# Kernel optimization log

Hardware: AMD Instinct MI355X
Metric: run time of the kernel (lower is better)

## Reference

```python
import jax, jax.numpy as jnp
import numpy as np

N, IN, M = 8192, 512, 512


def setup_inputs() -> dict:
    key = jax.random.key(0)
    ks = jax.random.split(key, 16)
    sI = 1.0 / np.sqrt(IN)
    sM = 1.0 / np.sqrt(M)
    def p(k, shape, scale):
        return jax.random.uniform(k, shape, jnp.float32, -scale, scale)
    # topologically sorted tree: parent[i] < i for i>0; root (i=0) points to sentinel N
    rng = np.random.default_rng(0)
    parent = (rng.random(N) * np.arange(N)).astype(np.int64)
    parent[0] = N
    return {
        "inputs": jax.random.normal(ks[0], (N, IN), jnp.float32),
        "parent": jnp.asarray(parent),
        # FPChildSumTreeLSTM params (bottom-up)
        "cs_Wx": p(ks[1], (5 * M, IN), sI), "cs_bx": p(ks[2], (5 * M,), sI),
        "cs_Wio": p(ks[3], (2 * M, M), sM), "cs_bio": p(ks[4], (2 * M,), sM),
        "cs_Wfz": p(ks[5], (2 * M, M), sM), "cs_bfz": p(ks[6], (2 * M,), sM),
        "cs_Wum": p(ks[7], (M, M), sM), "cs_bum": p(ks[8], (M,), sM),
        # FPChainTreeLSTM params (top-down)
        "ch_Wx": p(ks[9], (5 * M, IN), sI), "ch_bx": p(ks[10], (5 * M,), sI),
        "ch_Wh": p(ks[11], (4 * M, M), sM), "ch_bh": p(ks[12], (4 * M,), sM),
        "ch_Wum": p(ks[13], (M, M), sM), "ch_bum": p(ks[14], (M,), sM),
    }


def _childsum(inputs, parent, Wx, bx, Wio, bio, Wfz, bfz, Wum, bum):
    # Precompute input projections for all nodes at once; row N is a zero sentinel.
    px = inputs @ Wx.T + bx                                  # (N, 5M)
    px = jnp.concatenate([px, jnp.zeros((1, 5 * M), px.dtype)], axis=0)
    ix, fx, ox, zx, ux = (px[:, j * M:(j + 1) * M] for j in range(5))
    # Process nodes leaves->root (reverse topo order). Each finished node j
    # scatters its parent-dependent contributions into accumulators at parent[j]:
    #   acc_h  += h_j
    #   acc_fc += sigmoid(fx_parent + U_f h_j + b_f) * c_j
    #   acc_zc += sigmoid(zx_parent + U_z h_j + b_z) * tanh(c_j)
    # Leaves see zero accumulators, which exactly matches the torch zero phantom child.
    zero = jnp.zeros((N + 1, M), inputs.dtype)

    def step(carry, i):
        acc_h, acc_fc, acc_zc = carry
        io = acc_h[i] @ Wio.T + bio                          # (2M,)
        i_g = jax.nn.sigmoid(ix[i] + io[:M])
        o_g = jax.nn.sigmoid(ox[i] + io[M:])
        u = jnp.tanh(ux[i] + acc_zc[i] @ Wum.T + bum)
        c = i_g * u + acc_fc[i]
        h = o_g * jnp.tanh(c)
        p = parent[i]                                        # root -> sentinel N
        fz = h @ Wfz.T + bfz
        f = jax.nn.sigmoid(fx[p] + fz[:M])
        z = jax.nn.sigmoid(zx[p] + fz[M:])
        acc_h = acc_h.at[p].add(h)
        acc_fc = acc_fc.at[p].add(f * c)
        acc_zc = acc_zc.at[p].add(z * jnp.tanh(c))
        return (acc_h, acc_fc, acc_zc), h

    _, hs = jax.lax.scan(step, (zero, zero, zero), jnp.arange(N - 1, -1, -1))
    return hs[-1]                                            # root hidden, (M,)


def _chain(inputs, parent, Wx, bx, Wh, bh, Wum, bum):
    qx = inputs @ Wx.T + bx                                  # (N, 5M), order i,o,f,z,u
    ix, ox, fx, zx, ux = (qx[:, j * M:(j + 1) * M] for j in range(5))
    zero = jnp.zeros((N + 1, M), inputs.dtype)               # slot N = root's zero parent

    def step(carry, i):
        c_all, h_all = carry
        p = parent[i]
        pc, ph = c_all[p], h_all[p]
        g = ph @ Wh.T + bh                                   # (4M,), order i,o,f,z
        i_g = jax.nn.sigmoid(ix[i] + g[:M])
        o_g = jax.nn.sigmoid(ox[i] + g[M:2 * M])
        f_g = jax.nn.sigmoid(fx[i] + g[2 * M:3 * M])
        z_g = jax.nn.sigmoid(zx[i] + g[3 * M:])
        u = jnp.tanh(ux[i] + (z_g * jnp.tanh(pc)) @ Wum.T + bum)
        c = i_g * u + f_g * pc
        h = o_g * jnp.tanh(c)
        return (c_all.at[i].set(c), h_all.at[i].set(h)), None

    (_, h_all), _ = jax.lax.scan(step, (zero, zero), jnp.arange(N))
    return jnp.max(h_all[:N], axis=0)                        # max over all node hiddens, (M,)


def reference(inputs, parent, cs_Wx, cs_bx, cs_Wio, cs_bio, cs_Wfz, cs_bfz,
              cs_Wum, cs_bum, ch_Wx, ch_bx, ch_Wh, ch_bh, ch_Wum, ch_bum):
    frep = _childsum(inputs, parent, cs_Wx, cs_bx, cs_Wio, cs_bio,
                     cs_Wfz, cs_bfz, cs_Wum, cs_bum)
    brep = _chain(inputs, parent, ch_Wx, ch_bx, ch_Wh, ch_bh, ch_Wum, ch_bum)
    return jnp.concatenate([frep, brep])[None, :]            # (1, 2M)
```

## Files before the change

### kernel.cpp

```cpp
#include <hip/hip_runtime.h>
#include <hip/hip_cooperative_groups.h>
#include <hip/hip_bf16.h>

typedef unsigned short u16;
typedef unsigned int u32;
typedef unsigned long long u64;

#define NN 8192
#define PXC 2560
#define MAXD 36
#define GY 64
#define GYM 32

typedef __attribute__((ext_vector_type(8))) short bf16x8;
typedef __attribute__((ext_vector_type(4))) float f32x4;

static constexpr size_t SZ_PX  = (size_t)(NN + 1) * PXC * 2;
static constexpr size_t SZ_ACC = (size_t)(NN + 1) * 512 * 4;
static constexpr size_t SZ_HB  = (size_t)(NN + 1) * 512 * 2;
static constexpr size_t SZ_G   = (size_t)(NN + 1) * 1536 * 4;
static constexpr size_t SZ_NW  = (size_t)5242880 * 2;

static constexpr size_t OFF_PX    = 0;
static constexpr size_t OFF_QX    = OFF_PX + SZ_PX;
static constexpr size_t OFF_ACCH  = OFF_QX + SZ_PX;
static constexpr size_t OFF_ACCF  = OFF_ACCH + SZ_ACC;
static constexpr size_t OFF_ACCZ  = OFF_ACCF + SZ_ACC;
static constexpr size_t OFF_C     = OFF_ACCZ + SZ_ACC;
static constexpr size_t OFF_HB    = OFF_C + SZ_ACC;
static constexpr size_t OFF_ZB    = OFF_HB + SZ_HB;
static constexpr size_t OFF_G     = OFF_ZB + SZ_HB;
static constexpr size_t OFF_NW    = OFF_G + SZ_G;
static constexpr size_t OFF_DEPTH = OFF_NW + SZ_NW;
static constexpr size_t OFF_ORDER = OFF_DEPTH + (size_t)NN * 4;
static constexpr size_t OFF_MISC  = OFF_ORDER + (size_t)NN * 4;
static constexpr size_t OFF_LVL   = OFF_MISC + 1024;
static constexpr size_t OFF_NB    = OFF_LVL + 512;
static constexpr size_t OFF_PN    = OFF_NB + 20480;
static constexpr size_t OFF_PMAX  = OFF_PN + (size_t)NN * 4;
static constexpr size_t OFF_BAR   = OFF_PMAX + (size_t)128 * 512 * 4;
static constexpr size_t WS_TOTAL  = OFF_BAR + 32768;

#define NW_CSWX  0
#define NW_CHWX  1310720
#define NW_CSWIO 2621440
#define NW_CSWFZ 3145728
#define NW_CSWUM 3670016
#define NW_CHWH  3932160
#define NW_CHWUM 4980736

#define NB_CSBX  0
#define NB_CSBIO 2560
#define NB_CSBFZ 3584
#define NB_CSBUM 4608
#define NB_CHBX  5120
#define NB_CHBH  7680
#define NB_CHBUM 9728

__device__ __forceinline__ float bfu(u16 u) { return __uint_as_float(((u32)u) << 16); }
__device__ __forceinline__ u16 f2bf(float f) {
    u32 u = __float_as_uint(f);
    u += 0x7fffu + ((u >> 16) & 1u);
    return (u16)(u >> 16);
}
__device__ __forceinline__ float sigf(float x) {
    x = fminf(fmaxf(x, -30.f), 30.f);
    return 1.f / (1.f + __expf(-x));
}
__device__ __forceinline__ float tanhq(float x) {
    x = fminf(fmaxf(x, -15.f), 15.f);
    return 1.f - 2.f / (__expf(2.f * x) + 1.f);
}
__device__ __forceinline__ bf16x8 cvt8(const float* p) {
    float4 a = *(const float4*)p;
    float4 b = *(const float4*)(p + 4);
    union { u32 u[4]; bf16x8 v; } r;
    r.u[0] = ((__float_as_uint(a.x) + 0x8000u) >> 16) | ((__float_as_uint(a.y) + 0x8000u) & 0xffff0000u);
    r.u[1] = ((__float_as_uint(a.z) + 0x8000u) >> 16) | ((__float_as_uint(a.w) + 0x8000u) & 0xffff0000u);
    r.u[2] = ((__float_as_uint(b.x) + 0x8000u) >> 16) | ((__float_as_uint(b.y) + 0x8000u) & 0xffff0000u);
    r.u[3] = ((__float_as_uint(b.z) + 0x8000u) >> 16) | ((__float_as_uint(b.w) + 0x8000u) & 0xffff0000u);
    return r.v;
}

__device__ __forceinline__ u64 cld64(const void* p) {
    return __hip_atomic_load((const u64*)p, __ATOMIC_RELAXED, __HIP_MEMORY_SCOPE_AGENT);
}
__device__ __forceinline__ float cldf(const float* p) {
    return __hip_atomic_load(p, __ATOMIC_RELAXED, __HIP_MEMORY_SCOPE_AGENT);
}
__device__ __forceinline__ void cstf(float* p, float v) {
    __hip_atomic_store(p, v, __ATOMIC_RELAXED, __HIP_MEMORY_SCOPE_AGENT);
}
__device__ __forceinline__ void cst16(u16* p, u16 v) {
    __hip_atomic_store(p, v, __ATOMIC_RELAXED, __HIP_MEMORY_SCOPE_AGENT);
}
__device__ __forceinline__ bf16x8 cvt8a(const float* p) {
    union { u64 u; u32 w[2]; } a, b, c, d;
    a.u = cld64(p); b.u = cld64(p + 2); c.u = cld64(p + 4); d.u = cld64(p + 6);
    union { u32 u[4]; bf16x8 v; } r;
    r.u[0] = ((a.w[0] + 0x8000u) >> 16) | ((a.w[1] + 0x8000u) & 0xffff0000u);
    r.u[1] = ((b.w[0] + 0x8000u) >> 16) | ((b.w[1] + 0x8000u) & 0xffff0000u);
    r.u[2] = ((c.w[0] + 0x8000u) >> 16) | ((c.w[1] + 0x8000u) & 0xffff0000u);
    r.u[3] = ((d.w[0] + 0x8000u) >> 16) | ((d.w[1] + 0x8000u) & 0xffff0000u);
    return r.v;
}

__device__ __forceinline__ void grid_bar(u32* B, int bid, u32 tgt) {
    __syncthreads();
    int tid = threadIdx.x;
    if (tid == 0)
        __hip_atomic_store(B + 16 + bid * 16, tgt, __ATOMIC_RELAXED, __HIP_MEMORY_SCOPE_AGENT);
    if (blockIdx.x == 0) {
        if (tid < 256) {
            while (__hip_atomic_load(B + 16 + tid * 16, __ATOMIC_RELAXED, __HIP_MEMORY_SCOPE_AGENT) < tgt)
                __builtin_amdgcn_s_sleep(2);
        }
        __syncthreads();
        if (tid == 0)
            __hip_atomic_store(B, tgt, __ATOMIC_RELAXED, __HIP_MEMORY_SCOPE_AGENT);
    }
    if (tid == 0) {
        while (__hip_atomic_load(B, __ATOMIC_RELAXED, __HIP_MEMORY_SCOPE_AGENT) < tgt)
            __builtin_amdgcn_s_sleep(2);
        asm volatile("" ::: "memory");
    }
    __syncthreads();
}

__device__ __forceinline__ void mini_bar(u32* MF, int cgi, u32 tgt) {
    __syncthreads();
    if (threadIdx.x == 0) {
        __hip_atomic_store(MF + cgi * 4, tgt, __ATOMIC_RELAXED, __HIP_MEMORY_SCOPE_AGENT);
        for (;;) {
            u32 a = __hip_atomic_load(MF + 0,  __ATOMIC_RELAXED, __HIP_MEMORY_SCOPE_AGENT);
            u32 b = __hip_atomic_load(MF + 4,  __ATOMIC_RELAXED, __HIP_MEMORY_SCOPE_AGENT);
            u32 c = __hip_atomic_load(MF + 8,  __ATOMIC_RELAXED, __HIP_MEMORY_SCOPE_AGENT);
            u32 d = __hip_atomic_load(MF + 12, __ATOMIC_RELAXED, __HIP_MEMORY_SCOPE_AGENT);
            if (a >= tgt && b >= tgt && c >= tgt && d >= tgt) break;
            __builtin_amdgcn_s_sleep(1);
        }
        asm volatile("" ::: "memory");
    }
    __syncthreads();
}

__global__ void k_detect(const u32* __restrict__ fin, const u32* __restrict__ pin,
                         int* __restrict__ fcnt, int* __restrict__ pcnt,
                         u32* __restrict__ barz) {
    int i = blockIdx.x * 256 + threadIdx.x;
    if (i < 8192) barz[i] = 0u;
    if (i < 4096) {
        u32 w = fin[i];
        int e = (w >> 7) & 0xFF;
        if (w != 0u && e >= 0x70 && e <= 0x8F) atomicAdd(fcnt, 1);
    }
    if (i >= 1 && i < 4096) {
        if (pin[2 * i - 1] != 0u) atomicAdd(pcnt, 1);
    }
}

__global__ void k_pnorm_depth(const u32* __restrict__ pin, const int* __restrict__ pcnt,
                              int* __restrict__ pnorm, int* __restrict__ depth,
                              u16* __restrict__ HB, float* __restrict__ Call) {
    int i = blockIdx.x * 256 + threadIdx.x;
    if (i < 512) {
        HB[(size_t)NN * 512 + i] = 0;
        Call[(size_t)NN * 512 + i] = 0.f;
    }
    if (i >= NN) return;
    bool is64 = (*pcnt < 100);
    int p = (int)(is64 ? pin[2 * i] : pin[i]);
    pnorm[i] = p;
    int d = 0;
    while (p != NN && p >= 0 && p < NN && d < 9000) {
        d++;
        p = (int)(is64 ? pin[2 * p] : pin[p]);
    }
    depth[i] = d;
}

__global__ __launch_bounds__(1024) void k_levels(const int* __restrict__ depth,
                                                 int* __restrict__ lvl, int* __restrict__ order) {
    __shared__ int cnts[64];
    __shared__ int cur[64];
    int t = threadIdx.x;
    if (t < 64) cnts[t] = 0;
    __syncthreads();
    for (int i = t; i < NN; i += 1024) {
        int d = depth[i]; if (d > 63) d = 63;
        atomicAdd(&cnts[d], 1);
    }
    __syncthreads();
    if (t == 0) {
        int s = 0; lvl[0] = 0;
        for (int d = 0; d < 64; ++d) { cur[d] = s; s += cnts[d]; lvl[d + 1] = s; }
        int D = 1;
        for (int d = 63; d >= 0; --d) if (cnts[d] > 0) { D = d + 1; break; }
        lvl[80] = D;
    }
    __syncthreads();
    for (int i = t; i < NN; i += 1024) {
        int d = depth[i]; if (d > 63) d = 63;
        int pos = atomicAdd(&cur[d], 1);
        order[pos] = i;
    }
}

struct NormSrcs { const void* p[15]; };
__global__ __launch_bounds__(256) void k_norm_all(NormSrcs s, u16* __restrict__ NGI,
                                                  u16* __restrict__ NW, u16* __restrict__ NB,
                                                  const int* __restrict__ fcnt) {
    const int cum[16] = {0, 1048576, 1376256, 1703936, 1835008, 1966080, 2031616, 2293760,
                         2359296, 2359936, 2360192, 2360448, 2360576, 2361216, 2361728, 2361856};
    const int dof[15] = {0, NW_CSWX / 4, NW_CHWX / 4, NW_CSWIO / 4, NW_CSWFZ / 4, NW_CSWUM / 4,
                         NW_CHWH / 4, NW_CHWUM / 4, NB_CSBX / 4, NB_CSBIO / 4, NB_CSBFZ / 4,
                         NB_CSBUM / 4, NB_CHBX / 4, NB_CHBH / 4, NB_CHBUM / 4};
    bool isbf = (*fcnt > 2048);
    int total = 2361856;
    int istart = isbf ? cum[8] : 0;
    for (int i = istart + blockIdx.x * 256 + threadIdx.x; i < total; i += gridDim.x * 256) {
        int seg = 0;
#pragma unroll
        for (int k = 1; k < 15; ++k) if (i >= cum[k]) seg = k;
        int off = i - cum[seg];
        u16* dbase = (seg == 0) ? NGI : (seg < 8 ? NW : NB);
        ushort4* dst = (ushort4*)dbase + dof[seg] + off;
        if (isbf) {
            *dst = ((const ushort4*)s.p[seg])[off];
        } else {
            float4 v = ((const float4*)s.p[seg])[off];
            ushort4 o; o.x = f2bf(v.x); o.y = f2bf(v.y); o.z = f2bf(v.z); o.w = f2bf(v.w);
            *dst = o;
        }
    }
}

#define ASTR 528
__global__ __launch_bounds__(256) void k_gemm_in(
    const u16* __restrict__ Ao, const u16* __restrict__ An,
    const u16* __restrict__ Wcs_o, const u16* __restrict__ Wcs_n,
    const u16* __restrict__ Wch_o, const u16* __restrict__ Wch_n,
    const u16* __restrict__ bcs, const u16* __restrict__ bch,
    u16* __restrict__ Ccs, u16* __restrict__ Cch,
    const int* __restrict__ fcnt)
{
    __shared__ __align__(16) u16 AS[64 * ASTR];
    bool isbf = (*fcnt > 2048);
    int z = blockIdx.z;
    const u16* A = isbf ? Ao : An;
    const u16* W = z ? (isbf ? Wch_o : Wch_n) : (isbf ? Wcs_o : Wcs_n);
    const u16* bias = z ? bch : bcs;
    u16* C = z ? Cch : Ccs;

    int m0 = blockIdx.y * 64;
    for (int e = threadIdx.x; e < 64 * 64; e += 256) {
        int row = e >> 6, c8 = e & 63;
        *(uint4*)&AS[row * ASTR + c8 * 8] = *(const uint4*)(A + (size_t)(m0 + row) * 512 + c8 * 8);
    }
    __syncthreads();

    int wv = threadIdx.x >> 6;
    int lane = threadIdx.x & 63;
    int r = lane & 15, q = lane >> 4;
    int n0 = blockIdx.x * 256 + wv * 64;
    const u16* pb[4];
#pragma unroll
    for (int jt = 0; jt < 4; ++jt) pb[jt] = W + (size_t)(n0 + jt * 16 + r) * 512 + q * 8;
    f32x4 acc[4][4] = {};
#pragma unroll 2
    for (int k0 = 0; k0 < 512; k0 += 32) {
        bf16x8 a[4], b[4];
#pragma unroll
        for (int mi = 0; mi < 4; ++mi)
            a[mi] = *(const bf16x8*)&AS[(mi * 16 + r) * ASTR + k0 + q * 8];
#pragma unroll
        for (int jt = 0; jt < 4; ++jt) b[jt] = *(const bf16x8*)(pb[jt] + k0);
#pragma unroll
        for (int mi = 0; mi < 4; ++mi)
#pragma unroll
            for (int jt = 0; jt < 4; ++jt)
                acc[mi][jt] = __builtin_amdgcn_mfma_f32_16x16x32_bf16(a[mi], b[jt], acc[mi][jt], 0, 0, 0);
    }
#pragma unroll
    for (int jt = 0; jt < 4; ++jt) {
        int c = n0 + jt * 16 + r;
        float bv = bfu(bias[c]);
#pragma unroll
        for (int mi = 0; mi < 4; ++mi) {
            size_t b0 = (size_t)(m0 + mi * 16 + q * 4) * PXC + c;
#pragma unroll
            for (int i = 0; i < 4; ++i)
                C[b0 + (size_t)i * PXC] = f2bf(acc[mi][jt][i] + bv);
        }
    }
}

__global__ __launch_bounds__(512, 2) void comb_mega6(
    const int* __restrict__ order, const int* __restrict__ lvl, const int* __restrict__ parent,
    float* __restrict__ acc_h, float* __restrict__ acc_fc, float* __restrict__ acc_zc,
    const u16* __restrict__ Wio_o, const u16* __restrict__ Wio_n,
    const u16* __restrict__ Wum_o, const u16* __restrict__ Wum_n,
    const u16* __restrict__ Wfz_o, const u16* __restrict__ Wfz_n,
    const u16* __restrict__ bio, const u16* __restrict__ bum, const u16* __restrict__ bfz,
    const u16* __restrict__ px,
    u16* __restrict__ HB, float* __restrict__ Call,
    const u16* __restrict__ Wh_o, const u16* __restrict__ Wh_n,
    const u16* __restrict__ Wu2_o, const u16* __restrict__ Wu2_n,
    const u16* __restrict__ bh, const u16* __restrict__ bu2,
    const u16* __restrict__ qx, u16* __restrict__ ZB,
    float* __restrict__ G,
    void* __restrict__ outv, const int* __restrict__ fcnt,
    u32* __restrict__ BAR)
{
    __shared__ __align__(16) u16 LS[16384];
    __shared__ int ndl[16], pl[16];
    bool isbf = (*fcnt > 2048);
    int tid = threadIdx.x;
    int w = tid >> 6, lane = tid & 63;
    int r = lane & 15, q = lane >> 4;
    int rsw = (r & 7) << 4;
    int bid = blockIdx.x;
    int z = bid & 1;
    int cgi = (bid >> 1) & 3;
    int ty = bid >> 3;
    int col = (cgi * 8 + w) * 16 + r;
    u16* Gh = (u16*)G;
    char* LB = (char*)LS;
    int Dmax = lvl[80];
    u32* MF = BAR + 5120 + (size_t)((z << 5) + ty) * 16;
    u32 tgt = 0, mtgt = 0;

    const u16 *p1a, *p1b, *p1c, *p1d;
    const u16 *p2a, *p2b;
    float ba, bb, bc, bd, be;
    if (z == 0) {
        const u16* Wio = isbf ? Wio_o : Wio_n;
        const u16* Wum = isbf ? Wum_o : Wum_n;
        const u16* Wfz = isbf ? Wfz_o : Wfz_n;
        p1a = Wio + (size_t)col * 512 + q * 8;
        p1b = Wio + (size_t)(512 + col) * 512 + q * 8;
        p1c = Wum + (size_t)col * 512 + q * 8;
        p1d = p1c;
        p2a = Wfz + (size_t)col * 512 + q * 8;
        p2b = Wfz + (size_t)(512 + col) * 512 + q * 8;
        ba = bfu(bio[col]); bb = bfu(bio[512 + col]); bc = bfu(bum[col]);
        bd = bfu(bfz[col]); be = bfu(bfz[512 + col]);
    } else {
        const u16* Wh = isbf ? Wh_o : Wh_n;
        const u16* Wu = isbf ? Wu2_o : Wu2_n;
        p1a = Wh + (size_t)col * 512 + q * 8;
        p1b = Wh + (size_t)(512 + col) * 512 + q * 8;
        p1c = Wh + (size_t)(1024 + col) * 512 + q * 8;
        p1d = Wh + (size_t)(1536 + col) * 512 + q * 8;
        p2a = Wu + (size_t)col * 512 + q * 8;
        p2b = p2a;
        ba = bfu(bh[col]); bb = bfu(bh[512 + col]);
        bc = bfu(bh[1024 + col]); bd = bfu(bh[1536 + col]);
        be = bfu(bu2[col]);
    }

    for (int it = 0; it < Dmax; ++it) {
        int d = z ? it : (Dmax - 1 - it);
        int start = lvl[d], cnt = lvl[d + 1] - start;
        int ntiles = (cnt + 15) >> 4;

        for (int tile = ty; tile < ntiles; tile += GYM) {
            __syncthreads();
            if (tid < 16) {
                int tr = tile * 16 + tid;
                int nd = (tr < cnt) ? order[start + tr] : -1;
                ndl[tid] = nd;
                pl[tid] = (nd >= 0) ? parent[nd] : NN;
            }
            __syncthreads();

            if (z == 0) {
                for (int e = tid; e < 1024; e += 512) {
                    int slot = e >> 6, c8 = e & 63;
                    int nd = ndl[slot]; int nn = (nd < 0) ? NN : nd;
                    int boff = slot * 1024 + ((c8 * 16) ^ ((slot & 7) << 4));
                    *(bf16x8*)(LB + boff) = cvt8a(acc_h + (size_t)nn * 512 + c8 * 8);
                    *(bf16x8*)(LB + 16384 + boff) = cvt8a(acc_zc + (size_t)nn * 512 + c8 * 8);
                }
                __syncthreads();
                f32x4 ai = {}, ao = {}, au = {};
#pragma unroll 4
                for (int ko = 0; ko < 512; ko += 32) {
                    int abo = ((ko + q * 8) * 2) ^ rsw;
                    bf16x8 ah = *(const bf16x8*)(LB + r * 1024 + abo);
                    bf16x8 az = *(const bf16x8*)(LB + 16384 + r * 1024 + abo);
                    ai = __builtin_amdgcn_mfma_f32_16x16x32_bf16(ah, *(const bf16x8*)(p1a + ko), ai, 0, 0, 0);
                    ao = __builtin_amdgcn_mfma_f32_16x16x32_bf16(ah, *(const bf16x8*)(p1b + ko), ao, 0, 0, 0);
                    au = __builtin_amdgcn_mfma_f32_16x16x32_bf16(az, *(const bf16x8*)(p1c + ko), au, 0, 0, 0);
                }
                float ccv[4];
#pragma unroll
                for (int i2 = 0; i2 < 4; ++i2) {
                    int slot = q * 4 + i2;
                    int ni = ndl[slot];
                    ccv[i2] = 0.f;
                    if (ni < 0) continue;
                    int p = pl[slot];
                    size_t pxb = (size_t)ni * PXC, nb = (size_t)ni * 512;
                    float ig = sigf(bfu(px[pxb + col]) + ai[i2] + ba);
                    float og = sigf(bfu(px[pxb + 1024 + col]) + ao[i2] + bb);
                    float uu = tanhq(bfu(px[pxb + 2048 + col]) + au[i2] + bc);
                    float cc = ig * uu + cldf(acc_fc + nb + col);
                    float h = og * tanhq(cc);
                    ccv[i2] = cc;
                    cst16(&Gh[(size_t)ni * 3072 + 1024 + col], f2bf(h));
                    atomicAdd(&acc_h[(size_t)p * 512 + col], h);
                    if (ni == 0) {
                        if (isbf) ((u16*)outv)[col] = f2bf(h);
                        else ((float*)outv)[col] = h;
                    }
                }
                ++mtgt; mini_bar(MF, cgi, mtgt);
                for (int e = tid; e < 1024; e += 512) {
                    int slot = e >> 6, c8 = e & 63;
                    int nd = ndl[slot]; int nn = (nd < 0) ? NN : nd;
                    int boff = slot * 1024 + ((c8 * 16) ^ ((slot & 7) << 4));
                    *(bf16x8*)(LB + boff) = *(const bf16x8*)(Gh + (size_t)nn * 3072 + 1024 + c8 * 8);
                }
                __syncthreads();
                f32x4 af0 = {}, af1 = {}, az0 = {}, az1 = {};
#pragma unroll 4
                for (int ko = 0; ko < 256; ko += 32) {
                    int ab0 = ((ko + q * 8) * 2) ^ rsw;
                    int ab1 = ((ko + 256 + q * 8) * 2) ^ rsw;
                    bf16x8 h0 = *(const bf16x8*)(LB + r * 1024 + ab0);
                    bf16x8 h1 = *(const bf16x8*)(LB + r * 1024 + ab1);
                    af0 = __builtin_amdgcn_mfma_f32_16x16x32_bf16(h0, *(const bf16x8*)(p2a + ko), af0, 0, 0, 0);
                    az0 = __builtin_amdgcn_mfma_f32_16x16x32_bf16(h0, *(const bf16x8*)(p2b + ko), az0, 0, 0, 0);
                    af1 = __builtin_amdgcn_mfma_f32_16x16x32_bf16(h1, *(const bf16x8*)(p2a + 256 + ko), af1, 0, 0, 0);
                    az1 = __builtin_amdgcn_mfma_f32_16x16x32_bf16(h1, *(const bf16x8*)(p2b + 256 + ko), az1, 0, 0, 0);
                }
                f32x4 af = af0 + af1, az = az0 + az1;
#pragma unroll
                for (int i2 = 0; i2 < 4; ++i2) {
                    int slot = q * 4 + i2;
                    int ni = ndl[slot];
                    if (ni < 0) continue;
                    int p = pl[slot];
                    size_t pb = (size_t)p * 512, ppx = (size_t)p * PXC;
                    float cT = ccv[i2];
                    float f = sigf(bfu(px[ppx + 512 + col]) + af[i2] + bd);
                    atomicAdd(&acc_fc[pb + col], f * cT);
                    float zf = sigf(bfu(px[ppx + 1536 + col]) + az[i2] + be);
                    atomicAdd(&acc_zc[pb + col], zf * tanhq(cT));
                }
            } else {
                for (int e = tid; e < 1024; e += 512) {
                    int slot = e >> 6, c8 = e & 63;
                    int boff = slot * 1024 + ((c8 * 16) ^ ((slot & 7) << 4));
                    *(bf16x8*)(LB + boff) = *(const bf16x8*)(HB + (size_t)pl[slot] * 512 + c8 * 8);
                }
                __syncthreads();
                f32x4 gi = {}, go = {}, gf = {}, gz = {};
#pragma unroll 4
                for (int ko = 0; ko < 512; ko += 32) {
                    int abo = ((ko + q * 8) * 2) ^ rsw;
                    bf16x8 a = *(const bf16x8*)(LB + r * 1024 + abo);
                    gi = __builtin_amdgcn_mfma_f32_16x16x32_bf16(a, *(const bf16x8*)(p1a + ko), gi, 0, 0, 0);
                    go = __builtin_amdgcn_mfma_f32_16x16x32_bf16(a, *(const bf16x8*)(p1b + ko), go, 0, 0, 0);
                    gf = __builtin_amdgcn_mfma_f32_16x16x32_bf16(a, *(const bf16x8*)(p1c + ko), gf, 0, 0, 0);
                    gz = __builtin_amdgcn_mfma_f32_16x16x32_bf16(a, *(const bf16x8*)(p1d + ko), gz, 0, 0, 0);
                }
                float siR[4], soR[4], sfR[4], pcR[4];
#pragma unroll
                for (int i2 = 0; i2 < 4; ++i2) {
                    int slot = q * 4 + i2;
                    int ni = ndl[slot];
                    siR[i2] = 0.f; soR[i2] = 0.f; sfR[i2] = 0.f; pcR[i2] = 0.f;
                    if (ni < 0) continue;
                    int p = pl[slot];
                    size_t qb = (size_t)ni * PXC, nb = (size_t)ni * 512;
                    float si = sigf(bfu(qx[qb + col]) + gi[i2] + ba);
                    float so = sigf(bfu(qx[qb + 512 + col]) + go[i2] + bb);
                    float sf = sigf(bfu(qx[qb + 1024 + col]) + gf[i2] + bc);
                    float zg = sigf(bfu(qx[qb + 1536 + col]) + gz[i2] + bd);
                    float pc = Call[(size_t)p * 512 + col];
                    siR[i2] = si; soR[i2] = so; sfR[i2] = sf; pcR[i2] = pc;
                    cst16(&ZB[nb + col], f2bf(zg * tanhq(pc)));
                }
                ++mtgt; mini_bar(MF, cgi, mtgt);
                for (int e = tid; e < 1024; e += 512) {
                    int slot = e >> 6, c8 = e & 63;
                    int nd = ndl[slot]; int nn = (nd < 0) ? NN : nd;
                    int boff = slot * 1024 + ((c8 * 16) ^ ((slot & 7) << 4));
                    *(bf16x8*)(LB + boff) = *(const bf16x8*)(ZB + (size_t)nn * 512 + c8 * 8);
                }
                __syncthreads();
                f32x4 a0 = {}, a1 = {}, a2 = {}, a3 = {};
#pragma unroll 4
                for (int ko = 0; ko < 128; ko += 32) {
                    int b0 = ((ko + q * 8) * 2) ^ rsw;
                    int b1 = ((ko + 128 + q * 8) * 2) ^ rsw;
                    int b2 = ((ko + 256 + q * 8) * 2) ^ rsw;
                    int b3 = ((ko + 384 + q * 8) * 2) ^ rsw;
                    a0 = __builtin_amdgcn_mfma_f32_16x16x32_bf16(*(const bf16x8*)(LB + r * 1024 + b0),
                                                                 *(const bf16x8*)(p2a + ko), a0, 0, 0, 0);
                    a1 = __builtin_amdgcn_mfma_f32_16x16x32_bf16(*(const bf16x8*)(LB + r * 1024 + b1),
                                                                 *(const bf16x8*)(p2a + 128 + ko), a1, 0, 0, 0);
                    a2 = __builtin_amdgcn_mfma_f32_16x16x32_bf16(*(const bf16x8*)(LB + r * 1024 + b2),
                                                                 *(const bf16x8*)(p2a + 256 + ko), a2, 0, 0, 0);
                    a3 = __builtin_amdgcn_mfma_f32_16x16x32_bf16(*(const bf16x8*)(LB + r * 1024 + b3),
                                                                 *(const bf16x8*)(p2a + 384 + ko), a3, 0, 0, 0);
                }
                f32x4 au = (a0 + a1) + (a2 + a3);
#pragma unroll
                for (int i2 = 0; i2 < 4; ++i2) {
                    int slot = q * 4 + i2;
                    int ni = ndl[slot];
                    if (ni < 0) continue;
                    size_t qb = (size_t)ni * PXC, nb = (size_t)ni * 512;
                    float uu = tanhq(bfu(qx[qb + 2048 + col]) + au[i2] + be);
                    float cc = siR[i2] * uu + sfR[i2] * pcR[i2];
                    float h = soR[i2] * tanhq(cc);
                    cstf(&Call[nb + col], cc);
                    cst16(&HB[nb + col], f2bf(h));
                }
            }
        }
        ++tgt; grid_bar(BAR, bid, tgt);
    }
}

__global__ __launch_bounds__(512) void comb_s1(
    int iter,
    const int* __restrict__ order, const int* __restrict__ lvl, const int* __restrict__ parent,
    float* acc_h, const float* __restrict__ acc_fc, const float* __restrict__ acc_zc,
    const u16* __restrict__ Wio_o, const u16* __restrict__ Wio_n,
    const u16* __restrict__ Wum_o, const u16* __restrict__ Wum_n,
    const u16* __restrict__ bio, const u16* __restrict__ bum,
    const u16* __restrict__ px,
    const u16* __restrict__ HB, const float* __restrict__ Call,
    const u16* __restrict__ Wh_o, const u16* __restrict__ Wh_n,
    const u16* __restrict__ bh,
    const u16* __restrict__ qx, u16* __restrict__ ZB,
    float* __restrict__ G,
    void* __restrict__ outv, const int* __restrict__ fcnt)
{
    __shared__ __align__(16) u16 LS[16384];
    __shared__ int ndl[16], pl[16];
    bool isbf = (*fcnt > 2048);
    int tid = threadIdx.x;
    int w = tid >> 6, lane = tid & 63;
    int r = lane & 15, q = lane >> 4;
    int rsw = (r & 7) << 4;
    int col = (blockIdx.x * 8 + w) * 16 + r;
    u16* Gh = (u16*)G;
    char* LB = (char*)LS;
    int Dmax = lvl[80];
    int d = blockIdx.z ? iter : (Dmax - 1 - iter);
    if (d < 0 || d >= Dmax) return;
    int start = lvl[d], cnt = lvl[d + 1] - start;
    if (cnt <= 0) return;
    int ntiles = (cnt + 15) >> 4;

    if (blockIdx.z == 0) {
        const u16* Wio = isbf ? Wio_o : Wio_n;
        const u16* Wum = isbf ? Wum_o : Wum_n;
        const u16* pbi = Wio + (size_t)col * 512 + q * 8;
        const u16* pbo = Wio + (size_t)(512 + col) * 512 + q * 8;
        const u16* pbu = Wum + (size_t)col * 512 + q * 8;
        for (int tile = blockIdx.y; tile < ntiles; tile += GY) {
            __syncthreads();
            if (tid < 16) {
                int tr = tile * 16 + tid;
                int nd = (tr < cnt) ? order[start + tr] : -1;
                ndl[tid] = nd;
                pl[tid] = (nd >= 0) ? parent[nd] : NN;
            }
            __syncthreads();
            for (int e = tid; e < 1024; e += 512) {
                int slot = e >> 6, c8 = e & 63;
                int nd = ndl[slot]; int nn = (nd < 0) ? NN : nd;
                int boff = slot * 1024 + ((c8 * 16) ^ ((slot & 7) << 4));
                *(bf16x8*)(LB + boff) = cvt8(acc_h + (size_t)nn * 512 + c8 * 8);
                *(bf16x8*)(LB + 16384 + boff) = cvt8(acc_zc + (size_t)nn * 512 + c8 * 8);
            }
            __syncthreads();
            f32x4 ai = {}, ao = {}, au = {};
#pragma unroll 4
            for (int ko = 0; ko < 512; ko += 32) {
                int abo = ((ko + q * 8) * 2) ^ rsw;
                bf16x8 ah = *(const bf16x8*)(LB + r * 1024 + abo);
                bf16x8 az = *(const bf16x8*)(LB + 16384 + r * 1024 + abo);
                ai = __builtin_amdgcn_mfma_f32_16x16x32_bf16(ah, *(const bf16x8*)(pbi + ko), ai, 0, 0, 0);
                ao = __builtin_amdgcn_mfma_f32_16x16x32_bf16(ah, *(const bf16x8*)(pbo + ko), ao, 0, 0, 0);
                au = __builtin_amdgcn_mfma_f32_16x16x32_bf16(az, *(const bf16x8*)(pbu + ko), au, 0, 0, 0);
            }
            float bi_ = bfu(bio[col]), bo_ = bfu(bio[512 + col]), bu_ = bfu(bum[col]);
#pragma unroll
            for (int i2 = 0; i2 < 4; ++i2) {
                int slot = q * 4 + i2;
                int ni = ndl[slot];
                if (ni < 0) continue;
                int p = pl[slot];
                size_t pxb = (size_t)ni * PXC, nb = (size_t)ni * 512;
                float ig = sigf(bfu(px[pxb + col]) + ai[i2] + bi_);
                float og = sigf(bfu(px[pxb + 1024 + col]) + ao[i2] + bo_);
                float uu = tanhq(bfu(px[pxb + 2048 + col]) + au[i2] + bu_);
                float cc = ig * uu + acc_fc[nb + col];
                float h = og * tanhq(cc);
                G[(size_t)ni * 1536 + col] = cc;
                Gh[(size_t)ni * 3072 + 1024 + col] = f2bf(h);
                atomicAdd(&acc_h[(size_t)p * 512 + col], h);
                if (ni == 0) {
                    if (isbf) ((u16*)outv)[col] = f2bf(h);
                    else ((float*)outv)[col] = h;
                }
            }
        }
    } else {
        const u16* Wh = isbf ? Wh_o : Wh_n;
        const u16* pbi = Wh + (size_t)col * 512 + q * 8;
        const u16* pbo = Wh + (size_t)(512 + col) * 512 + q * 8;
        const u16* pbf = Wh + (size_t)(1024 + col) * 512 + q * 8;
        const u16* pbz = Wh + (size_t)(1536 + col) * 512 + q * 8;
        for (int tile = blockIdx.y; tile < ntiles; tile += GY) {
            __syncthreads();
            if (tid < 16) {
                int tr = tile * 16 + tid;
                int nd = (tr < cnt) ? order[start + tr] : -1;
                ndl[tid] = nd;
                pl[tid] = (nd >= 0) ? parent[nd] : NN;
            }
            __syncthreads();
            for (int e = tid; e < 1024; e += 512) {
                int slot = e >> 6, c8 = e & 63;
                int boff = slot * 1024 + ((c8 * 16) ^ ((slot & 7) << 4));
                *(bf16x8*)(LB + boff) = *(const bf16x8*)(HB + (size_t)pl[slot] * 512 + c8 * 8);
            }
            __syncthreads();
            f32x4 gi = {}, go = {}, gf = {}, gz = {};
#pragma unroll 4
            for (int ko = 0; ko < 512; ko += 32) {
                int abo = ((ko + q * 8) * 2) ^ rsw;
                bf16x8 a = *(const bf16x8*)(LB + r * 1024 + abo);
                gi = __builtin_amdgcn_mfma_f32_16x16x32_bf16(a, *(const bf16x8*)(pbi + ko), gi, 0, 0, 0);
                go = __builtin_amdgcn_mfma_f32_16x16x32_bf16(a, *(const bf16x8*)(pbo + ko), go, 0, 0, 0);
                gf = __builtin_amdgcn_mfma_f32_16x16x32_bf16(a, *(const bf16x8*)(pbf + ko), gf, 0, 0, 0);
                gz = __builtin_amdgcn_mfma_f32_16x16x32_bf16(a, *(const bf16x8*)(pbz + ko), gz, 0, 0, 0);
            }
            float bi_ = bfu(bh[col]), bo_ = bfu(bh[512 + col]);
            float bf_ = bfu(bh[1024 + col]), bz_ = bfu(bh[1536 + col]);
#pragma unroll
            for (int i2 = 0; i2 < 4; ++i2) {
                int slot = q * 4 + i2;
                int ni = ndl[slot];
                if (ni < 0) continue;
                int p = pl[slot];
                size_t qb = (size_t)ni * PXC, gb = (size_t)ni * 1536, nb = (size_t)ni * 512;
                float si = sigf(bfu(qx[qb + col]) + gi[i2] + bi_);
                float so = sigf(bfu(qx[qb + 512 + col]) + go[i2] + bo_);
                float sf = sigf(bfu(qx[qb + 1024 + col]) + gf[i2] + bf_);
                float zg = sigf(bfu(qx[qb + 1536 + col]) + gz[i2] + bz_);
                G[gb + col] = si;
                G[gb + 512 + col] = so;
                G[gb + 1024 + col] = sf;
                ZB[nb + col] = f2bf(zg * tanhq(Call[(size_t)p * 512 + col]));
            }
        }
    }
}

__global__ __launch_bounds__(512) void comb_s2(
    int iter,
// ... 84 lines not shown
                ndl[tid] = nd;
                pl[tid] = (nd >= 0) ? parent[nd] : NN;
            }
            __syncthreads();
            for (int e = tid; e < 1024; e += 512) {
                int slot = e >> 6, c8 = e & 63;
                int nd = ndl[slot]; int nn = (nd < 0) ? NN : nd;
                int boff = slot * 1024 + ((c8 * 16) ^ ((slot & 7) << 4));
                *(bf16x8*)(LB + boff) = *(const bf16x8*)(ZB + (size_t)nn * 512 + c8 * 8);
            }
            __syncthreads();
            f32x4 a0 = {}, a1 = {}, a2 = {}, a3 = {};
#pragma unroll 4
            for (int ko = 0; ko < 128; ko += 32) {
                int b0 = ((ko + q * 8) * 2) ^ rsw;
                int b1 = ((ko + 128 + q * 8) * 2) ^ rsw;
                int b2 = ((ko + 256 + q * 8) * 2) ^ rsw;
                int b3 = ((ko + 384 + q * 8) * 2) ^ rsw;
                a0 = __builtin_amdgcn_mfma_f32_16x16x32_bf16(*(const bf16x8*)(LB + r * 1024 + b0),
                                                             *(const bf16x8*)(pbu + ko), a0, 0, 0, 0);
                a1 = __builtin_amdgcn_mfma_f32_16x16x32_bf16(*(const bf16x8*)(LB + r * 1024 + b1),
                                                             *(const bf16x8*)(pbu + 128 + ko), a1, 0, 0, 0);
                a2 = __builtin_amdgcn_mfma_f32_16x16x32_bf16(*(const bf16x8*)(LB + r * 1024 + b2),
                                                             *(const bf16x8*)(pbu + 256 + ko), a2, 0, 0, 0);
                a3 = __builtin_amdgcn_mfma_f32_16x16x32_bf16(*(const bf16x8*)(LB + r * 1024 + b3),
                                                             *(const bf16x8*)(pbu + 384 + ko), a3, 0, 0, 0);
            }
            f32x4 au = (a0 + a1) + (a2 + a3);
            float bu_ = bfu(bum[col]);
#pragma unroll
            for (int i2 = 0; i2 < 4; ++i2) {
                int slot = q * 4 + i2;
                int ni = ndl[slot];
                if (ni < 0) continue;
                int p = pl[slot];
                size_t qb = (size_t)ni * PXC, gb = (size_t)ni * 1536, nb = (size_t)ni * 512;
                float uu = tanhq(bfu(qx[qb + 2048 + col]) + au[i2] + bu_);
                float si = G[gb + col];
                float so = G[gb + 512 + col];
                float sf = G[gb + 1024 + col];
                float pc = Call[(size_t)p * 512 + col];
                float cc = si * uu + sf * pc;
                float h = so * tanhq(cc);
                Call[nb + col] = cc;
                HB[nb + col] = f2bf(h);
            }
        }
    }
}

__global__ __launch_bounds__(256) void k_maxA(const u16* __restrict__ HB, float* __restrict__ pmax) {
    int b = blockIdx.x, t = threadIdx.x;
    float m1 = -1e30f, m2 = -1e30f;
    for (int rr = b * 128; rr < b * 128 + 128; ++rr) {
        m1 = fmaxf(m1, bfu(HB[(size_t)rr * 512 + t]));
        m2 = fmaxf(m2, bfu(HB[(size_t)rr * 512 + t + 256]));
    }
    pmax[(size_t)b * 512 + t] = m1; pmax[(size_t)b * 512 + t + 256] = m2;
}
__global__ void k_maxB(const float* __restrict__ pmax, void* __restrict__ outv,
                       const int* __restrict__ fcnt) {
    int j = threadIdx.x;
    float m = -1e30f;
    for (int b = 0; b < 64; ++b) m = fmaxf(m, pmax[(size_t)b * 512 + j]);
    bool isbf = (*fcnt > 2048);
    if (isbf) ((u16*)outv)[512 + j] = f2bf(m);
    else ((float*)outv)[512 + j] = m;
}

__global__ void k_wsfail(u16* out) {
    int i = blockIdx.x * 256 + threadIdx.x;
    if (i < 1024) out[i] = f2bf(12345.f);
}

extern "C" void kernel_launch(void* const* d_in, const int* in_sizes, int n_in,
                              void* d_out, int out_size, void* d_ws, size_t ws_size,
                              hipStream_t stream) {
    char* base = (char*)d_ws;
    u16* px = (u16*)(base + OFF_PX);
    u16* qx = (u16*)(base + OFF_QX);
    float* acc_h = (float*)(base + OFF_ACCH);
    float* acc_fc = (float*)(base + OFF_ACCF);
    float* acc_zc = (float*)(base + OFF_ACCZ);
    float* Call = (float*)(base + OFF_C);
    u16* HB = (u16*)(base + OFF_HB);
    u16* ZB = (u16*)(base + OFF_ZB);
    float* G = (float*)(base + OFF_G);
    u16* NGI = (u16*)(base + OFF_G);
    u16* NW = (u16*)(base + OFF_NW);
    int* depth = (int*)(base + OFF_DEPTH);
    int* order = (int*)(base + OFF_ORDER);
    int* counts = (int*)(base + OFF_MISC);
    int* fcnt = counts + 128;
    int* pcnt = counts + 129;
    int* lvl = (int*)(base + OFF_LVL);
    u16* NB = (u16*)(base + OFF_NB);
    int* pnorm = (int*)(base + OFF_PN);
    float* pmax = (float*)(base + OFF_PMAX);
    u32* BAR = (u32*)(base + OFF_BAR);

    const u16* in_bf   = (const u16*)d_in[0];
    const u16* csWx_o  = (const u16*)d_in[2];
    const u16* csWio_o = (const u16*)d_in[4];
    const u16* csWfz_o = (const u16*)d_in[6];
    const u16* csWum_o = (const u16*)d_in[8];
    const u16* chWx_o  = (const u16*)d_in[10];
    const u16* chWh_o  = (const u16*)d_in[12];
    const u16* chWum_o = (const u16*)d_in[14];

    if (ws_size < WS_TOTAL) { k_wsfail<<<4, 256, 0, stream>>>((u16*)d_out); return; }

    hipMemsetAsync(base + OFF_MISC, 0, 1024, stream);
    hipMemsetAsync(base + OFF_ACCH, 0, 3 * SZ_ACC, stream);

    k_detect<<<32, 256, 0, stream>>>((const u32*)d_in[0], (const u32*)d_in[1], fcnt, pcnt, BAR);
    k_pnorm_depth<<<32, 256, 0, stream>>>((const u32*)d_in[1], pcnt, pnorm, depth, HB, Call);
    k_levels<<<1, 1024, 0, stream>>>(depth, lvl, order);

    NormSrcs srcs;
    srcs.p[0] = d_in[0];  srcs.p[1] = d_in[2];  srcs.p[2] = d_in[10]; srcs.p[3] = d_in[4];
    srcs.p[4] = d_in[6];  srcs.p[5] = d_in[8];  srcs.p[6] = d_in[12]; srcs.p[7] = d_in[14];
    srcs.p[8] = d_in[3];  srcs.p[9] = d_in[5];  srcs.p[10] = d_in[7]; srcs.p[11] = d_in[9];
    srcs.p[12] = d_in[11]; srcs.p[13] = d_in[13]; srcs.p[14] = d_in[15];
    k_norm_all<<<2048, 256, 0, stream>>>(srcs, NGI, NW, NB, fcnt);

    dim3 gg(PXC / 256, NN / 64, 2);
    k_gemm_in<<<gg, 256, 0, stream>>>(in_bf, NGI,
                                      csWx_o, NW + NW_CSWX, chWx_o, NW + NW_CHWX,
                                      NB + NB_CSBX, NB + NB_CHBX, px, qx, fcnt);

    {
        const u16* nWio = NW + NW_CSWIO; const u16* nWum = NW + NW_CSWUM;
        const u16* nWfz = NW + NW_CSWFZ; const u16* nWh = NW + NW_CHWH;
        const u16* nWu2 = NW + NW_CHWUM;
        const u16* b_io = NB + NB_CSBIO; const u16* b_um = NB + NB_CSBUM;
        const u16* b_fz = NB + NB_CSBFZ; const u16* b_h = NB + NB_CHBH;
        const u16* b_u2 = NB + NB_CHBUM;
        const int* order_c = order; const int* lvl_c = lvl; const int* par_c = pnorm;
        const u16* px_c = px; const u16* qx_c = qx;
        void* outp = d_out; const int* fcnt_c = fcnt;
        u32* bar_c = BAR;
        void* margs[] = {
            (void*)&order_c, (void*)&lvl_c, (void*)&par_c,
            (void*)&acc_h, (void*)&acc_fc, (void*)&acc_zc,
            (void*)&csWio_o, (void*)&nWio, (void*)&csWum_o, (void*)&nWum,
            (void*)&csWfz_o, (void*)&nWfz,
            (void*)&b_io, (void*)&b_um, (void*)&b_fz,
            (void*)&px_c, (void*)&HB, (void*)&Call,
            (void*)&chWh_o, (void*)&nWh, (void*)&chWum_o, (void*)&nWu2,
            (void*)&b_h, (void*)&b_u2,
            (void*)&qx_c, (void*)&ZB, (void*)&G,
            (void*)&outp, (void*)&fcnt_c, (void*)&bar_c
        };
        hipError_t ce = hipLaunchCooperativeKernel((const void*)comb_mega6,
                                                   dim3(256), dim3(512), margs, 0, stream);
        if (ce != hipSuccess) {
            (void)hipGetLastError();
            dim3 gl(4, GY, 2);
            for (int i = 0; i < MAXD; ++i) {
                comb_s1<<<gl, 512, 0, stream>>>(i, order, lvl, pnorm,
                                                acc_h, acc_fc, acc_zc,
                                                csWio_o, NW + NW_CSWIO, csWum_o, NW + NW_CSWUM,
                                                NB + NB_CSBIO, NB + NB_CSBUM, px,
                                                HB, Call, chWh_o, NW + NW_CHWH, NB + NB_CHBH,
                                                qx, ZB, G, d_out, fcnt);
                comb_s2<<<gl, 512, 0, stream>>>(i, order, lvl, pnorm,
                                                csWfz_o, NW + NW_CSWFZ, NB + NB_CSBFZ, px,
                                                acc_fc, acc_zc,
                                                ZB, qx, chWum_o, NW + NW_CHWUM, NB + NB_CHBUM,
                                                Call, HB, G, fcnt);
            }
        }
    }

    k_maxA<<<64, 256, 0, stream>>>(HB, pmax);
    k_maxB<<<1, 512, 0, stream>>>(pmax, d_out, fcnt);
}
```

Before: 1.221 ms.

## Replace inter-block mini barriers with redundant full-width gate compute per block

Each of the four column-group blocks now computes all 512 columns of the first-stage gate matmul itself, instead of computing 128 columns and exchanging results through global memory. The full intermediate vector (h for child-sum, z*tanh(pc) for chain) is written straight into LDS, which removes the mini_bar spin-wait and the global round-trip between the two matmul phases. The cost is four times the first-stage MFMA work and weight traffic per block, more accumulator registers, and a larger LDS footprint. The launch-bounds occupancy hint of 2 is also dropped.

```diff
diff --git a/kernel.cpp b/kernel.cpp
--- a/kernel.cpp
+++ b/kernel.cpp
@@ -127,23 +127,6 @@
     __syncthreads();
 }
 
-__device__ __forceinline__ void mini_bar(u32* MF, int cgi, u32 tgt) {
-    __syncthreads();
-    if (threadIdx.x == 0) {
-        __hip_atomic_store(MF + cgi * 4, tgt, __ATOMIC_RELAXED, __HIP_MEMORY_SCOPE_AGENT);
-        for (;;) {
-            u32 a = __hip_atomic_load(MF + 0,  __ATOMIC_RELAXED, __HIP_MEMORY_SCOPE_AGENT);
-            u32 b = __hip_atomic_load(MF + 4,  __ATOMIC_RELAXED, __HIP_MEMORY_SCOPE_AGENT);
-            u32 c = __hip_atomic_load(MF + 8,  __ATOMIC_RELAXED, __HIP_MEMORY_SCOPE_AGENT);
-            u32 d = __hip_atomic_load(MF + 12, __ATOMIC_RELAXED, __HIP_MEMORY_SCOPE_AGENT);
-            if (a >= tgt && b >= tgt && c >= tgt && d >= tgt) break;
-            __builtin_amdgcn_s_sleep(1);
-        }
-        asm volatile("" ::: "memory");
-    }
-    __syncthreads();
-}
-
 __global__ void k_detect(const u32* __restrict__ fin, const u32* __restrict__ pin,
                          int* __restrict__ fcnt, int* __restrict__ pcnt,
                          u32* __restrict__ barz) {
@@ -295,7 +278,7 @@
     }
 }
 
-__global__ __launch_bounds__(512, 2) void comb_mega6(
+__global__ __launch_bounds__(512) void comb_mega7(
     const int* __restrict__ order, const int* __restrict__ lvl, const int* __restrict__ parent,
     float* __restrict__ acc_h, float* __restrict__ acc_fc, float* __restrict__ acc_zc,
     const u16* __restrict__ Wio_o, const u16* __restrict__ Wio_n,
@@ -312,7 +295,7 @@
     void* __restrict__ outv, const int* __restrict__ fcnt,
     u32* __restrict__ BAR)
 {
-    __shared__ __align__(16) u16 LS[16384];
+    __shared__ __align__(16) u16 LS[24576];
     __shared__ int ndl[16], pl[16];
     bool isbf = (*fcnt > 2048);
     int tid = threadIdx.x;
@@ -323,40 +306,49 @@
     int z = bid & 1;
     int cgi = (bid >> 1) & 3;
     int ty = bid >> 3;
-    int col = (cgi * 8 + w) * 16 + r;
-    u16* Gh = (u16*)G;
+    int colw = w * 16 + r;
+    int col = colw + cgi * 128;
     char* LB = (char*)LS;
     int Dmax = lvl[80];
-    u32* MF = BAR + 5120 + (size_t)((z << 5) + ty) * 16;
-    u32 tgt = 0, mtgt = 0;
+    u32 tgt = 0;
 
     const u16 *p1a, *p1b, *p1c, *p1d;
     const u16 *p2a, *p2b;
-    float ba, bb, bc, bd, be;
+    float b1a[4], b1b[4], b1c[4], b1d[4];
+    float bd, be;
     if (z == 0) {
         const u16* Wio = isbf ? Wio_o : Wio_n;
         const u16* Wum = isbf ? Wum_o : Wum_n;
         const u16* Wfz = isbf ? Wfz_o : Wfz_n;
-        p1a = Wio + (size_t)col * 512 + q * 8;
-        p1b = Wio + (size_t)(512 + col) * 512 + q * 8;
-        p1c = Wum + (size_t)col * 512 + q * 8;
+        p1a = Wio + (size_t)colw * 512 + q * 8;
+        p1b = Wio + (size_t)(512 + colw) * 512 + q * 8;
+        p1c = Wum + (size_t)colw * 512 + q * 8;
         p1d = p1c;
         p2a = Wfz + (size_t)col * 512 + q * 8;
         p2b = Wfz + (size_t)(512 + col) * 512 + q * 8;
-        ba = bfu(bio[col]); bb = bfu(bio[512 + col]); bc = bfu(bum[col]);
+#pragma unroll
+        for (int f = 0; f < 4; ++f) {
+            int cf = colw + f * 128;
+            b1a[f] = bfu(bio[cf]); b1b[f] = bfu(bio[512 + cf]); b1c[f] = bfu(bum[cf]);
+            b1d[f] = 0.f;
+        }
         bd = bfu(bfz[col]); be = bfu(bfz[512 + col]);
     } else {
         const u16* Wh = isbf ? Wh_o : Wh_n;
         const u16* Wu = isbf ? Wu2_o : Wu2_n;
-        p1a = Wh + (size_t)col * 512 + q * 8;
-        p1b = Wh + (size_t)(512 + col) * 512 + q * 8;
-        p1c = Wh + (size_t)(1024 + col) * 512 + q * 8;
-        p1d = Wh + (size_t)(1536 + col) * 512 + q * 8;
+        p1a = Wh + (size_t)colw * 512 + q * 8;
+        p1b = Wh + (size_t)(512 + colw) * 512 + q * 8;
+        p1c = Wh + (size_t)(1024 + colw) * 512 + q * 8;
+        p1d = Wh + (size_t)(1536 + colw) * 512 + q * 8;
         p2a = Wu + (size_t)col * 512 + q * 8;
         p2b = p2a;
-        ba = bfu(bh[col]); bb = bfu(bh[512 + col]);
-        bc = bfu(bh[1024 + col]); bd = bfu(bh[1536 + col]);
-        be = bfu(bu2[col]);
+#pragma unroll
+        for (int f = 0; f < 4; ++f) {
+            int cf = colw + f * 128;
+            b1a[f] = bfu(bh[cf]); b1b[f] = bfu(bh[512 + cf]);
+            b1c[f] = bfu(bh[1024 + cf]); b1d[f] = bfu(bh[1536 + cf]);
+        }
+        bd = 0.f; be = bfu(bu2[col]);
     }
 
     for (int it = 0; it < Dmax; ++it) {
@@ -383,15 +375,18 @@
                     *(bf16x8*)(LB + 16384 + boff) = cvt8a(acc_zc + (size_t)nn * 512 + c8 * 8);
                 }
                 __syncthreads();
-                f32x4 ai = {}, ao = {}, au = {};
-#pragma unroll 4
+                f32x4 ai[4] = {}, ao[4] = {}, au[4] = {};
+#pragma unroll 2
                 for (int ko = 0; ko < 512; ko += 32) {
                     int abo = ((ko + q * 8) * 2) ^ rsw;
                     bf16x8 ah = *(const bf16x8*)(LB + r * 1024 + abo);
                     bf16x8 az = *(const bf16x8*)(LB + 16384 + r * 1024 + abo);
-                    ai = __builtin_amdgcn_mfma_f32_16x16x32_bf16(ah, *(const bf16x8*)(p1a + ko), ai, 0, 0, 0);
-                    ao = __builtin_amdgcn_mfma_f32_16x16x32_bf16(ah, *(const bf16x8*)(p1b + ko), ao, 0, 0, 0);
-                    au = __builtin_amdgcn_mfma_f32_16x16x32_bf16(az, *(const bf16x8*)(p1c + ko), au, 0, 0, 0);
+#pragma unroll
+                    for (int f = 0; f < 4; ++f) {
+                        ai[f] = __builtin_amdgcn_mfma_f32_16x16x32_bf16(ah, *(const bf16x8*)(p1a + f * 65536 + ko), ai[f], 0, 0, 0);
+                        ao[f] = __builtin_amdgcn_mfma_f32_16x16x32_bf16(ah, *(const bf16x8*)(p1b + f * 65536 + ko), ao[f], 0, 0, 0);
+                        au[f] = __builtin_amdgcn_mfma_f32_16x16x32_bf16(az, *(const bf16x8*)(p1c + f * 65536 + ko), au[f], 0, 0, 0);
+                    }
                 }
                 float ccv[4];
 #pragma unroll
@@ -402,25 +397,24 @@
                     if (ni < 0) continue;
                     int p = pl[slot];
                     size_t pxb = (size_t)ni * PXC, nb = (size_t)ni * 512;
-                    float ig = sigf(bfu(px[pxb + col]) + ai[i2] + ba);
-                    float og = sigf(bfu(px[pxb + 1024 + col]) + ao[i2] + bb);
-                    float uu = tanhq(bfu(px[pxb + 2048 + col]) + au[i2] + bc);
-                    float cc = ig * uu + cldf(acc_fc + nb + col);
-                    float h = og * tanhq(cc);
-                    ccv[i2] = cc;
-                    cst16(&Gh[(size_t)ni * 3072 + 1024 + col], f2bf(h));
-                    atomicAdd(&acc_h[(size_t)p * 512 + col], h);
-                    if (ni == 0) {
-                        if (isbf) ((u16*)outv)[col] = f2bf(h);
-                        else ((float*)outv)[col] = h;
+#pragma unroll
+                    for (int f = 0; f < 4; ++f) {
+                        int cf = colw + f * 128;
+                        float ig = sigf(bfu(px[pxb + cf]) + ai[f][i2] + b1a[f]);
+                        float og = sigf(bfu(px[pxb + 1024 + cf]) + ao[f][i2] + b1b[f]);
+                        float uu = tanhq(bfu(px[pxb + 2048 + cf]) + au[f][i2] + b1c[f]);
+                        float cc = ig * uu + cldf(acc_fc + nb + cf);
+                        float h = og * tanhq(cc);
+                        *(u16*)(LB + 32768 + slot * 1024 + ((cf * 2) ^ ((slot & 7) << 4))) = f2bf(h);
+                        if (f == cgi) {
+                            ccv[i2] = cc;
+                            atomicAdd(&acc_h[(size_t)p * 512 + cf], h);
+                            if (ni == 0) {
+                                if (isbf) ((u16*)outv)[cf] = f2bf(h);
+                                else ((float*)outv)[cf] = h;
+                            }
+                        }
                     }
-                }
-                ++mtgt; mini_bar(MF, cgi, mtgt);
-                for (int e = tid; e < 1024; e += 512) {
-                    int slot = e >> 6, c8 = e & 63;
-                    int nd = ndl[slot]; int nn = (nd < 0) ? NN : nd;
-                    int boff = slot * 1024 + ((c8 * 16) ^ ((slot & 7) << 4));
-                    *(bf16x8*)(LB + boff) = *(const bf16x8*)(Gh + (size_t)nn * 3072 + 1024 + c8 * 8);
                 }
                 __syncthreads();
                 f32x4 af0 = {}, af1 = {}, az0 = {}, az1 = {};
@@ -428,8 +422,8 @@
                 for (int ko = 0; ko < 256; ko += 32) {
                     int ab0 = ((ko + q * 8) * 2) ^ rsw;
                     int ab1 = ((ko + 256 + q * 8) * 2) ^ rsw;
-                    bf16x8 h0 = *(const bf16x8*)(LB + r * 1024 + ab0);
-                    bf16x8 h1 = *(const bf16x8*)(LB + r * 1024 + ab1);
+                    bf16x8 h0 = *(const bf16x8*)(LB + 32768 + r * 1024 + ab0);
+                    bf16x8 h1 = *(const bf16x8*)(LB + 32768 + r * 1024 + ab1);
                     af0 = __builtin_amdgcn_mfma_f32_16x16x32_bf16(h0, *(const bf16x8*)(p2a + ko), af0, 0, 0, 0);
                     az0 = __builtin_amdgcn_mfma_f32_16x16x32_bf16(h0, *(const bf16x8*)(p2b + ko), az0, 0, 0, 0);
                     af1 = __builtin_amdgcn_mfma_f32_16x16x32_bf16(h1, *(const bf16x8*)(p2a + 256 + ko), af1, 0, 0, 0);
@@ -456,15 +450,18 @@
                     *(bf16x8*)(LB + boff) = *(const bf16x8*)(HB + (size_t)pl[slot] * 512 + c8 * 8);
                 }
                 __syncthreads();
-                f32x4 gi = {}, go = {}, gf = {}, gz = {};
-#pragma unroll 4
+                f32x4 gi[4] = {}, go[4] = {}, gf[4] = {}, gz[4] = {};
+#pragma unroll 2
                 for (int ko = 0; ko < 512; ko += 32) {
                     int abo = ((ko + q * 8) * 2) ^ rsw;
                     bf16x8 a = *(const bf16x8*)(LB + r * 1024 + abo);
-                    gi = __builtin_amdgcn_mfma_f32_16x16x32_bf16(a, *(const bf16x8*)(p1a + ko), gi, 0, 0, 0);
-                    go = __builtin_amdgcn_mfma_f32_16x16x32_bf16(a, *(const bf16x8*)(p1b + ko), go, 0, 0, 0);
-                    gf = __builtin_amdgcn_mfma_f32_16x16x32_bf16(a, *(const bf16x8*)(p1c + ko), gf, 0, 0, 0);
-                    gz = __builtin_amdgcn_mfma_f32_16x16x32_bf16(a, *(const bf16x8*)(p1d + ko), gz, 0, 0, 0);
+#pragma unroll
+                    for (int f = 0; f < 4; ++f) {
+                        gi[f] = __builtin_amdgcn_mfma_f32_16x16x32_bf16(a, *(const bf16x8*)(p1a + f * 65536 + ko), gi[f], 0, 0, 0);
+                        go[f] = __builtin_amdgcn_mfma_f32_16x16x32_bf16(a, *(const bf16x8*)(p1b + f * 65536 + ko), go[f], 0, 0, 0);
+                        gf[f] = __builtin_amdgcn_mfma_f32_16x16x32_bf16(a, *(const bf16x8*)(p1c + f * 65536 + ko), gf[f], 0, 0, 0);
+                        gz[f] = __builtin_amdgcn_mfma_f32_16x16x32_bf16(a, *(const bf16x8*)(p1d + f * 65536 + ko), gz[f], 0, 0, 0);
+                    }
                 }
                 float siR[4], soR[4], sfR[4], pcR[4];
 #pragma unroll
@@ -474,21 +471,20 @@
                     siR[i2] = 0.f; soR[i2] = 0.f; sfR[i2] = 0.f; pcR[i2] = 0.f;
                     if (ni < 0) continue;
                     int p = pl[slot];
-                    size_t qb = (size_t)ni * PXC, nb = (size_t)ni * 512;
-                    float si = sigf(bfu(qx[qb + col]) + gi[i2] + ba);
-                    float so = sigf(bfu(qx[qb + 512 + col]) + go[i2] + bb);
-                    float sf = sigf(bfu(qx[qb + 1024 + col]) + gf[i2] + bc);
-                    float zg = sigf(bfu(qx[qb + 1536 + col]) + gz[i2] + bd);
-                    float pc = Call[(size_t)p * 512 + col];
-                    siR[i2] = si; soR[i2] = so; sfR[i2] = sf; pcR[i2] = pc;
-                    cst16(&ZB[nb + col], f2bf(zg * tanhq(pc)));
-                }
-                ++mtgt; mini_bar(MF, cgi, mtgt);
-                for (int e = tid; e < 1024; e += 512) {
-                    int slot = e >> 6, c8 = e & 63;
-                    int nd = ndl[slot]; int nn = (nd < 0) ? NN : nd;
-                    int boff = slot * 1024 + ((c8 * 16) ^ ((slot & 7) << 4));
-                    *(bf16x8*)(LB + boff) = *(const bf16x8*)(ZB + (size_t)nn * 512 + c8 * 8);
+                    size_t qb = (size_t)ni * PXC;
+#pragma unroll
+                    for (int f = 0; f < 4; ++f) {
+                        int cf = colw + f * 128;
+                        float zg = sigf(bfu(qx[qb + 1536 + cf]) + gz[f][i2] + b1d[f]);
+                        float pc = Call[(size_t)p * 512 + cf];
+                        *(u16*)(LB + 16384 + slot * 1024 + ((cf * 2) ^ ((slot & 7) << 4))) = f2bf(zg * tanhq(pc));
+                        if (f == cgi) {
+                            siR[i2] = sigf(bfu(qx[qb + cf]) + gi[f][i2] + b1a[f]);
+                            soR[i2] = sigf(bfu(qx[qb + 512 + cf]) + go[f][i2] + b1b[f]);
+                            sfR[i2] = sigf(bfu(qx[qb + 1024 + cf]) + gf[f][i2] + b1c[f]);
+                            pcR[i2] = pc;
+                        }
+                    }
                 }
                 __syncthreads();
                 f32x4 a0 = {}, a1 = {}, a2 = {}, a3 = {};
@@ -498,23 +494,23 @@
                     int b1 = ((ko + 128 + q * 8) * 2) ^ rsw;
                     int b2 = ((ko + 256 + q * 8) * 2) ^ rsw;
                     int b3 = ((ko + 384 + q * 8) * 2) ^ rsw;
-                    a0 = __builtin_amdgcn_mfma_f32_16x16x32_bf16(*(const bf16x8*)(LB + r * 1024 + b0),
+                    a0 = __builtin_amdgcn_mfma_f32_16x16x32_bf16(*(const bf16x8*)(LB + 16384 + r * 1024 + b0),
                                                                  *(const bf16x8*)(p2a + ko), a0, 0, 0, 0);
-                    a1 = __builtin_amdgcn_mfma_f32_16x16x32_bf16(*(const bf16x8*)(LB + r * 1024 + b1),
+                    a1 = __builtin_amdgcn_mfma_f32_16x16x32_bf16(*(const bf16x8*)(LB + 16384 + r * 1024 + b1),
                                                                  *(const bf16x8*)(p2a + 128 + ko), a1, 0, 0, 0);
-                    a2 = __builtin_amdgcn_mfma_f32_16x16x32_bf16(*(const bf16x8*)(LB + r * 1024 + b2),
+                    a2 = __builtin_amdgcn_mfma_f32_16x16x32_bf16(*(const bf16x8*)(LB + 16384 + r * 1024 + b2),
                                                                  *(const bf16x8*)(p2a + 256 + ko), a2, 0, 0, 0);
-                    a3 = __builtin_amdgcn_mfma_f32_16x16x32_bf16(*(const bf16x8*)(LB + r * 1024 + b3),
+                    a3 = __builtin_amdgcn_mfma_f32_16x16x32_bf16(*(const bf16x8*)(LB + 16384 + r * 1024 + b3),
                                                                  *(const bf16x8*)(p2a + 384 + ko), a3, 0, 0, 0);
                 }
-                f32x4 au = (a0 + a1) + (a2 + a3);
+                f32x4 auv = (a0 + a1) + (a2 + a3);
 #pragma unroll
                 for (int i2 = 0; i2 < 4; ++i2) {
                     int slot = q * 4 + i2;
                     int ni = ndl[slot];
                     if (ni < 0) continue;
                     size_t qb = (size_t)ni * PXC, nb = (size_t)ni * 512;
-                    float uu = tanhq(bfu(qx[qb + 2048 + col]) + au[i2] + be);
+                    float uu = tanhq(bfu(qx[qb + 2048 + col]) + auv[i2] + be);
                     float cc = siR[i2] * uu + sfR[i2] * pcR[i2];
                     float h = soR[i2] * tanhq(cc);
                     cstf(&Call[nb + col], cc);
@@ -905,7 +901,7 @@
             (void*)&qx_c, (void*)&ZB, (void*)&G,
             (void*)&outp, (void*)&fcnt_c, (void*)&bar_c
         };
-        hipError_t ce = hipLaunchCooperativeKernel((const void*)comb_mega6,
+        hipError_t ce = hipLaunchCooperativeKernel((const void*)comb_mega7,
                                                    dim3(256), dim3(512), margs, 0, stream);
         if (ce != hipSuccess) {
             (void)hipGetLastError();
```

After: 2.672 ms. 2.19x slower.
